# Kernel tuning notes

Measured on AMD Instinct MI355X. Metric: run time of the kernel, lower is better.

Reference implementation:

```python
import jax, jax.numpy as jnp
import numpy as np

DECAY = 0.8
CODEBOOK_SIZE = 1024
DIM = 128


def setup_inputs() -> dict:
    key = jax.random.key(0)
    k1, k2 = jax.random.split(key)
    x = jax.random.normal(k1, (16, 4096, DIM), dtype=jnp.float32)
    embed = jax.random.normal(k2, (CODEBOOK_SIZE, DIM), dtype=jnp.float32)
    ema_embed = embed * 1.0  # ema_num_initial = 1.0
    ema_num = jnp.ones((CODEBOOK_SIZE,), dtype=jnp.float32)
    return {"x": x, "embed": embed, "ema_embed": ema_embed, "ema_num": ema_num}


def reference(x, embed, ema_embed, ema_num):
    # flatten: [..., d] -> [N, d]
    shape = x.shape
    flatten = x.reshape(-1, shape[-1])  # [N, d]
    distance = -2.0 * (flatten @ embed.T) + jnp.sum(embed * embed, axis=-1)  # [N, K]
    embed_ind = jnp.argmin(distance, axis=-1)  # [N]
    quantize = embed[embed_ind.reshape(shape[:-1])]  # gather -> [..., d]

    # training branch: onehot^T @ flatten == segment_sum over code indices
    num_curr = jax.ops.segment_sum(
        jnp.ones_like(embed_ind, dtype=jnp.float32), embed_ind,
        num_segments=CODEBOOK_SIZE)  # [K]
    embed_curr = jax.ops.segment_sum(
        flatten.astype(jnp.float32), embed_ind,
        num_segments=CODEBOOK_SIZE)  # [K, d]

    ema_num_new = ema_num * DECAY + (1.0 - DECAY) * num_curr
    ema_embed_new = ema_embed * DECAY + (1.0 - DECAY) * embed_curr
    embed_new = ema_embed_new / ema_num_new[:, None]
    return quantize, embed_new, ema_embed_new, ema_num_new
```

## Files before the change

### kernel.cpp

```cpp
#include <hip/hip_runtime.h>

#define NPTS    65536
#define DIM     128
#define KCODES  1024
#define BM      64
#define TILE_C  64
#define NTHR    256
#define NTILE   (KCODES / TILE_C)

typedef _Float16 f16x8 __attribute__((ext_vector_type(8)));
typedef float    f32x4 __attribute__((ext_vector_type(4)));

__device__ __forceinline__ void gload_lds16(const void* g, void* l) {
    __builtin_amdgcn_global_load_lds(
        (const __attribute__((address_space(1))) void*)g,
        (__attribute__((address_space(3))) void*)l, 16, 0, 0);
}

__global__ __launch_bounds__(256)
void pack_kernel(const float* __restrict__ embed, _Float16* __restrict__ ebf,
                 int* __restrict__ ghist, int* __restrict__ gcursor,
                 const float* __restrict__ ema_embed, float* __restrict__ acc,
                 float* __restrict__ hn)
{
    __shared__ float partial[256];
    const int t = threadIdx.x;
    const int b = blockIdx.x;
    const int g = b * 256 + t;
    if (g < KCODES) { ghist[g] = 0; gcursor[g] = 0; }
    {
        float4 e0 = reinterpret_cast<const float4*>(ema_embed)[g];
        float4 e1 = reinterpret_cast<const float4*>(ema_embed)[g + 16384];
        reinterpret_cast<float4*>(acc)[g] =
            (float4){0.8f * e0.x, 0.8f * e0.y, 0.8f * e0.z, 0.8f * e0.w};
        reinterpret_cast<float4*>(acc)[g + 16384] =
            (float4){0.8f * e1.x, 0.8f * e1.y, 0.8f * e1.z, 0.8f * e1.w};
    }

    const int tc  = g >> 10;
    const int f   = (g >> 6) & 15;
    const int l   = g & 63;
    const int nt  = f >> 2;
    const int akk = f & 3;
    const int hg  = l >> 4;
    const int n   = l & 15;
    const int c   = tc * TILE_C + nt * 16 + n;
    const int d0  = akk * 32 + hg * 8;
    const float* src = embed + (long)c * DIM + d0;
    float4 v0 = *reinterpret_cast<const float4*>(src);
    float4 v1 = *reinterpret_cast<const float4*>(src + 4);
    float vv[8] = {v0.x, v0.y, v0.z, v0.w, v1.x, v1.y, v1.z, v1.w};
    f16x8 out;
    float ss = 0.f;
    #pragma unroll
    for (int j = 0; j < 8; ++j) {
        _Float16 h = (_Float16)vv[j];
        out[j] = h;
        float r = (float)h;
        ss += r * r;
    }
    *reinterpret_cast<f16x8*>(ebf + (long)g * 8) = out;

    partial[t] = ss;
    __syncthreads();
    if (t < 16) {
        float s = 0.f;
        #pragma unroll
        for (int k = 0; k < 16; ++k) s += partial[t + k * 16];
        hn[(b >> 2) * TILE_C + (b & 3) * 16 + t] = 0.5f * s;
    }
}

__global__ __launch_bounds__(NTHR, 4)
void argmin_kernel(const float* __restrict__ x, const _Float16* __restrict__ ebf,
                   const float* __restrict__ halfnorm, const float* __restrict__ embed,
                   int* __restrict__ ind, float* __restrict__ quant,
                   int* __restrict__ ghist)
{
    __shared__ _Float16 es[2][8192];
    __shared__ int      hist[KCODES];
    __shared__ int      bidx[BM];

    const int t    = threadIdx.x;
    const int lane = t & 63;
    const int w    = t >> 6;
    const int r16  = lane & 15;
    const int h4   = lane >> 4;
    const long xbase = (long)blockIdx.x * BM * DIM;
    const int  wp    = w * 16;

    for (int i = t; i < KCODES; i += NTHR) hist[i] = 0;

    f16x8 a[4];
    {
        const long prow = xbase + (long)(wp + r16) * DIM;
        #pragma unroll
        for (int akk = 0; akk < 4; ++akk) {
            const float* s = x + prow + akk * 32 + h4 * 8;
            float4 u0 = *reinterpret_cast<const float4*>(s);
            float4 u1 = *reinterpret_cast<const float4*>(s + 4);
            float vv[8] = {u0.x, u0.y, u0.z, u0.w, u1.x, u1.y, u1.z, u1.w};
            #pragma unroll
            for (int j = 0; j < 8; ++j) a[akk][j] = (_Float16)vv[j];
        }
    }

    #pragma unroll
    for (int i = 0; i < 4; ++i) {
        const int f = w * 4 + i;
        gload_lds16(ebf + (long)f * 512 + lane * 8, &es[0][f * 512]);
    }
    float hnv_cur[4], hnv_nxt[4];
    #pragma unroll
    for (int nt = 0; nt < 4; ++nt) hnv_cur[nt] = halfnorm[nt * 16 + r16];
    __syncthreads();

    float bestv[4];
    int   besti[4];
    #pragma unroll
    for (int s = 0; s < 4; ++s) { bestv[s] = -1e30f; besti[s] = 0; }

    #pragma unroll 1
    for (int tile = 0; tile < NTILE; ++tile) {
        if (tile + 1 < NTILE) {
            const long gbase = (long)(tile + 1) * 8192;
            #pragma unroll
            for (int i = 0; i < 4; ++i) {
                const int f = w * 4 + i;
                gload_lds16(ebf + gbase + f * 512 + lane * 8, &es[(tile + 1) & 1][f * 512]);
            }
            #pragma unroll
            for (int nt = 0; nt < 4; ++nt)
                hnv_nxt[nt] = halfnorm[(tile + 1) * TILE_C + nt * 16 + r16];
        }

        f32x4 C[4];
        #pragma unroll
        for (int nt = 0; nt < 4; ++nt) C[nt] = (f32x4){0.f, 0.f, 0.f, 0.f};

        #pragma unroll
        for (int akk = 0; akk < 4; ++akk) {
            #pragma unroll
            for (int nt = 0; nt < 4; ++nt) {
                f16x8 B = *reinterpret_cast<const f16x8*>(
                    &es[tile & 1][(nt * 4 + akk) * 512 + lane * 8]);
                C[nt] = __builtin_amdgcn_mfma_f32_16x16x32_f16(a[akk], B, C[nt], 0, 0, 0);
            }
        }

        #pragma unroll
        for (int nt = 0; nt < 4; ++nt) {
            const int c = tile * TILE_C + nt * 16 + r16;
            #pragma unroll
            for (int reg = 0; reg < 4; ++reg) {
                float sc = C[nt][reg] - hnv_cur[nt];
                if (sc > bestv[reg]) { bestv[reg] = sc; besti[reg] = c; }
            }
        }
        #pragma unroll
        for (int nt = 0; nt < 4; ++nt) hnv_cur[nt] = hnv_nxt[nt];
        __syncthreads();
    }

    #pragma unroll
    for (int s = 0; s < 4; ++s) {
        float v = bestv[s];
        int   i = besti[s];
        #pragma unroll
        for (int off = 1; off < 16; off <<= 1) {
            float ov = __shfl_xor(v, off);
            int   oi = __shfl_xor(i, off);
            if (ov > v || (ov == v && oi < i)) { v = ov; i = oi; }
        }
        bestv[s] = v; besti[s] = i;
    }
    if (r16 == 0) {
        #pragma unroll
        for (int s = 0; s < 4; ++s) {
            int p = wp + h4 * 4 + s;
            bidx[p] = besti[s];
            ind[blockIdx.x * BM + p] = besti[s];
        }
    }
    __syncthreads();

    if (t < BM) atomicAdd(&hist[bidx[t]], 1);

    float4* dst = reinterpret_cast<float4*>(quant + xbase);
    #pragma unroll
    for (int i = 0; i < 8; ++i) {
        int idx = i * NTHR + t;
        int p   = idx >> 5;
        int q   = idx & 31;
        int c   = bidx[p];
        dst[idx] = reinterpret_cast<const float4*>(embed + (long)c * DIM)[q];
    }

    __syncthreads();
    for (int i = t; i < KCODES; i += NTHR)
        if (hist[i]) atomicAdd(&ghist[i], hist[i]);
}

__global__ __launch_bounds__(256)
void scatter_kernel(const int* __restrict__ ghist, const int* __restrict__ ind,
                    const float* __restrict__ ema_num, float* __restrict__ ema_num_new,
                    int* __restrict__ gcursor, int* __restrict__ sorted,
                    int* __restrict__ scode)
{
    __shared__ int off_lds[KCODES];
    __shared__ int wsum[4];
    const int t    = threadIdx.x;
    const int lane = t & 63;
    const int w    = t >> 6;

    int v[4], pre[4];
    int s = 0;
    #pragma unroll
    for (int j = 0; j < 4; ++j) {
        v[j] = ghist[t * 4 + j];
        pre[j] = s;
        s += v[j];
    }
    int incl = s;
    #pragma unroll
    for (int off = 1; off < 64; off <<= 1) {
        int u = __shfl_up(incl, off);
        if (lane >= off) incl += u;
    }
    if (lane == 63) wsum[w] = incl;
    __syncthreads();
    if (t == 0) {
        int a = 0;
        #pragma unroll
        for (int k = 0; k < 4; ++k) { int tmp = wsum[k]; wsum[k] = a; a += tmp; }
    }
    __syncthreads();
    const int excl = wsum[w] + incl - s;
    #pragma unroll
    for (int j = 0; j < 4; ++j) off_lds[t * 4 + j] = excl + pre[j];

    if (blockIdx.x == 0) {
        #pragma unroll
        for (int j = 0; j < 4; ++j)
            ema_num_new[t * 4 + j] = ema_num[t * 4 + j] * 0.8f + 0.2f * (float)v[j];
    }
    __syncthreads();

    const int p = blockIdx.x * 256 + t;
    const int c = ind[p];
    const int pos = off_lds[c] + atomicAdd(&gcursor[c], 1);
    sorted[pos] = p;
    scode[pos]  = c;
}

__global__ __launch_bounds__(128)
void sum2_kernel(const float* __restrict__ x, const int* __restrict__ sorted,
                 const int* __restrict__ scode, float* __restrict__ acc)
{
    __shared__ int sp[64];
    __shared__ int sc[64];
    const int t = threadIdx.x;
    const int base = blockIdx.x * 64;
    if (t < 64) { sp[t] = sorted[base + t]; sc[t] = scode[base + t]; }
    __syncthreads();

    float a = 0.f;
    int cprev = sc[0];
    #pragma unroll 1
    for (int kk = 0; kk < 8; ++kk) {
        float v[8];
        #pragma unroll
        for (int i = 0; i < 8; ++i)
            v[i] = x[(long)sp[kk * 8 + i] * DIM + t];
        #pragma unroll
        for (int i = 0; i < 8; ++i) {
            const int c = sc[kk * 8 + i];
            if (c != cprev) {
                atomicAdd(&acc[(long)cprev * DIM + t], 0.2f * a);
                a = 0.f; cprev = c;
            }
            a += v[i];
        }
    }
    atomicAdd(&acc[(long)cprev * DIM + t], 0.2f * a);
}

__global__ __launch_bounds__(256)
void final_kernel(const float* __restrict__ acc, const float* __restrict__ ema_num_new,
                  float* __restrict__ embed_new)
{
    const int g = blockIdx.x * 256 + threadIdx.x;
    float4 v = reinterpret_cast<const float4*>(acc)[g];
    const float en = ema_num_new[g >> 5];
    float4 o = {v.x / en, v.y / en, v.z / en, v.w / en};
    reinterpret_cast<float4*>(embed_new)[g] = o;
}

extern "C" void kernel_launch(void* const* d_in, const int* in_sizes, int n_in,
                              void* d_out, int out_size, void* d_ws, size_t ws_size,
                              hipStream_t stream)
{
    const float* x         = (const float*)d_in[0];
    const float* embed     = (const float*)d_in[1];
    const float* ema_embed = (const float*)d_in[2];
    const float* ema_num   = (const float*)d_in[3];

    float* out0 = (float*)d_out;
    float* out1 = out0 + 8388608;
    float* out2 = out1 + 131072;
    float* out3 = out2 + 131072;

    char* ws = (char*)d_ws;
    float*    hn      = (float*)ws;
    int*      ind     = (int*)(ws + 4096);
    _Float16* ebf     = (_Float16*)(ws + 266240);
    int*      ghist   = (int*)(ws + 528384);
    int*      gcursor = (int*)(ws + 532480);
    int*      sorted  = (int*)(ws + 536576);
    int*      scode   = (int*)(ws + 798720);

    pack_kernel<<<64, 256, 0, stream>>>(embed, ebf, ghist, gcursor, ema_embed,
                                        out2, hn);
    argmin_kernel<<<NPTS / BM, NTHR, 0, stream>>>(x, ebf, hn, embed, ind, out0, ghist);
    scatter_kernel<<<NPTS / 256, 256, 0, stream>>>(ghist, ind, ema_num, out3,
                                                   gcursor, sorted, scode);
    sum2_kernel<<<NPTS / 64, 128, 0, stream>>>(x, sorted, scode, out2);
    final_kernel<<<128, 256, 0, stream>>>(out2, out3, out1);
}
```

Baseline: 95.96 us.

## Switch argmin GEMM to 32x32x16 MFMA with 128-row blocks

Replaces the 16x16x32 f16 MFMA tiles with 32x32x16 tiles, giving each wave 32 points and doubling the block to 128 rows. The packed codebook layout and the half-norm computation in the pack kernel are reworked to match. This halves how often each codebook tile is reloaded from LDS per point and cuts the number of blocks, but raises register use (16 accumulators plus 16 best values and indices), so launch bounds drop to 2 blocks per SIMD. The row-to-index mapping of the reduction changes accordingly, and a wrong mapping would give incorrect indices.

```diff
diff --git a/kernel.cpp b/kernel.cpp
--- a/kernel.cpp
+++ b/kernel.cpp
@@ -3,13 +3,13 @@
 #define NPTS    65536
 #define DIM     128
 #define KCODES  1024
-#define BM      64
+#define BM      128
 #define TILE_C  64
 #define NTHR    256
 #define NTILE   (KCODES / TILE_C)
 
-typedef _Float16 f16x8 __attribute__((ext_vector_type(8)));
-typedef float    f32x4 __attribute__((ext_vector_type(4)));
+typedef _Float16 f16x8  __attribute__((ext_vector_type(8)));
+typedef float    f32x16 __attribute__((ext_vector_type(16)));
 
 __device__ __forceinline__ void gload_lds16(const void* g, void* l) {
     __builtin_amdgcn_global_load_lds(
@@ -37,41 +37,49 @@
             (float4){0.8f * e1.x, 0.8f * e1.y, 0.8f * e1.z, 0.8f * e1.w};
     }
 
-    const int tc  = g >> 10;
-    const int f   = (g >> 6) & 15;
-    const int l   = g & 63;
-    const int nt  = f >> 2;
-    const int akk = f & 3;
-    const int hg  = l >> 4;
-    const int n   = l & 15;
-    const int c   = tc * TILE_C + nt * 16 + n;
-    const int d0  = akk * 32 + hg * 8;
-    const float* src = embed + (long)c * DIM + d0;
-    float4 v0 = *reinterpret_cast<const float4*>(src);
-    float4 v1 = *reinterpret_cast<const float4*>(src + 4);
-    float vv[8] = {v0.x, v0.y, v0.z, v0.w, v1.x, v1.y, v1.z, v1.w};
-    f16x8 out;
-    float ss = 0.f;
-    #pragma unroll
-    for (int j = 0; j < 8; ++j) {
-        _Float16 h = (_Float16)vv[j];
-        out[j] = h;
-        float r = (float)h;
-        ss += r * r;
-    }
-    *reinterpret_cast<f16x8*>(ebf + (long)g * 8) = out;
-
-    partial[t] = ss;
-    __syncthreads();
-    if (t < 16) {
-        float s = 0.f;
-        #pragma unroll
-        for (int k = 0; k < 16; ++k) s += partial[t + k * 16];
-        hn[(b >> 2) * TILE_C + (b & 3) * 16 + t] = 0.5f * s;
-    }
-}
-
-__global__ __launch_bounds__(NTHR, 4)
+    {
+        const int tc  = g >> 10;
+        const int f   = (g >> 6) & 15;
+        const int l   = g & 63;
+        const int nt  = f >> 3;
+        const int kc  = f & 7;
+        const int c   = tc * TILE_C + nt * 32 + (l & 31);
+        const int d0  = kc * 16 + (l >> 5) * 8;
+        const float* src = embed + (long)c * DIM + d0;
+        float4 v0 = *reinterpret_cast<const float4*>(src);
+        float4 v1 = *reinterpret_cast<const float4*>(src + 4);
+        float vv[8] = {v0.x, v0.y, v0.z, v0.w, v1.x, v1.y, v1.z, v1.w};
+        f16x8 out;
+        #pragma unroll
+        for (int j = 0; j < 8; ++j) out[j] = (_Float16)vv[j];
+        *reinterpret_cast<f16x8*>(ebf + (long)g * 8) = out;
+    }
+
+    {
+        const int c2    = b * 16 + (t >> 4);
+        const int chunk = t & 15;
+        const float* src = embed + (long)c2 * DIM + chunk * 8;
+        float4 v0 = *reinterpret_cast<const float4*>(src);
+        float4 v1 = *reinterpret_cast<const float4*>(src + 4);
+        float vv[8] = {v0.x, v0.y, v0.z, v0.w, v1.x, v1.y, v1.z, v1.w};
+        float ss = 0.f;
+        #pragma unroll
+        for (int j = 0; j < 8; ++j) {
+            float r = (float)(_Float16)vv[j];
+            ss += r * r;
+        }
+        partial[t] = ss;
+        __syncthreads();
+        if ((t & 15) == 0) {
+            float s = 0.f;
+            #pragma unroll
+            for (int j = 0; j < 16; ++j) s += partial[t + j];
+            hn[c2] = 0.5f * s;
+        }
+    }
+}
+
+__global__ __launch_bounds__(NTHR, 2)
 void argmin_kernel(const float* __restrict__ x, const _Float16* __restrict__ ebf,
                    const float* __restrict__ halfnorm, const float* __restrict__ embed,
                    int* __restrict__ ind, float* __restrict__ quant,
@@ -84,24 +92,24 @@
     const int t    = threadIdx.x;
     const int lane = t & 63;
     const int w    = t >> 6;
-    const int r16  = lane & 15;
-    const int h4   = lane >> 4;
+    const int r32  = lane & 31;
+    const int ksub = lane >> 5;
     const long xbase = (long)blockIdx.x * BM * DIM;
-    const int  wp    = w * 16;
+    const int  wp    = w * 32;
 
     for (int i = t; i < KCODES; i += NTHR) hist[i] = 0;
 
-    f16x8 a[4];
+    f16x8 a[8];
     {
-        const long prow = xbase + (long)(wp + r16) * DIM;
-        #pragma unroll
-        for (int akk = 0; akk < 4; ++akk) {
-            const float* s = x + prow + akk * 32 + h4 * 8;
+        const long prow = xbase + (long)(wp + r32) * DIM;
+        #pragma unroll
+        for (int kc = 0; kc < 8; ++kc) {
+            const float* s = x + prow + kc * 16 + ksub * 8;
             float4 u0 = *reinterpret_cast<const float4*>(s);
             float4 u1 = *reinterpret_cast<const float4*>(s + 4);
             float vv[8] = {u0.x, u0.y, u0.z, u0.w, u1.x, u1.y, u1.z, u1.w};
             #pragma unroll
-            for (int j = 0; j < 8; ++j) a[akk][j] = (_Float16)vv[j];
+            for (int j = 0; j < 8; ++j) a[kc][j] = (_Float16)vv[j];
         }
     }
 
@@ -110,15 +118,15 @@
         const int f = w * 4 + i;
         gload_lds16(ebf + (long)f * 512 + lane * 8, &es[0][f * 512]);
     }
-    float hnv_cur[4], hnv_nxt[4];
-    #pragma unroll
-    for (int nt = 0; nt < 4; ++nt) hnv_cur[nt] = halfnorm[nt * 16 + r16];
-    __syncthreads();
-
-    float bestv[4];
-    int   besti[4];
-    #pragma unroll
-    for (int s = 0; s < 4; ++s) { bestv[s] = -1e30f; besti[s] = 0; }
+    float hnv_cur[2], hnv_nxt[2];
+    #pragma unroll
+    for (int nt = 0; nt < 2; ++nt) hnv_cur[nt] = halfnorm[nt * 32 + r32];
+    __syncthreads();
+
+    float bestv[16];
+    int   besti[16];
+    #pragma unroll
+    for (int s = 0; s < 16; ++s) { bestv[s] = -1e30f; besti[s] = 0; }
 
     #pragma unroll 1
     for (int tile = 0; tile < NTILE; ++tile) {
@@ -130,54 +138,49 @@
                 gload_lds16(ebf + gbase + f * 512 + lane * 8, &es[(tile + 1) & 1][f * 512]);
             }
             #pragma unroll
-            for (int nt = 0; nt < 4; ++nt)
-                hnv_nxt[nt] = halfnorm[(tile + 1) * TILE_C + nt * 16 + r16];
-        }
-
-        f32x4 C[4];
-        #pragma unroll
-        for (int nt = 0; nt < 4; ++nt) C[nt] = (f32x4){0.f, 0.f, 0.f, 0.f};
-
-        #pragma unroll
-        for (int akk = 0; akk < 4; ++akk) {
-            #pragma unroll
-            for (int nt = 0; nt < 4; ++nt) {
+            for (int nt = 0; nt < 2; ++nt)
+                hnv_nxt[nt] = halfnorm[(tile + 1) * TILE_C + nt * 32 + r32];
+        }
+
+        #pragma unroll
+        for (int nt = 0; nt < 2; ++nt) {
+            f32x16 C = {0.f, 0.f, 0.f, 0.f, 0.f, 0.f, 0.f, 0.f,
+                        0.f, 0.f, 0.f, 0.f, 0.f, 0.f, 0.f, 0.f};
+            #pragma unroll
+            for (int kc = 0; kc < 8; ++kc) {
                 f16x8 B = *reinterpret_cast<const f16x8*>(
-                    &es[tile & 1][(nt * 4 + akk) * 512 + lane * 8]);
-                C[nt] = __builtin_amdgcn_mfma_f32_16x16x32_f16(a[akk], B, C[nt], 0, 0, 0);
+                    &es[tile & 1][(nt * 8 + kc) * 512 + lane * 8]);
+                C = __builtin_amdgcn_mfma_f32_32x32x16_f16(a[kc], B, C, 0, 0, 0);
             }
-        }
-
-        #pragma unroll
-        for (int nt = 0; nt < 4; ++nt) {
-            const int c = tile * TILE_C + nt * 16 + r16;
-            #pragma unroll
-            for (int reg = 0; reg < 4; ++reg) {
-                float sc = C[nt][reg] - hnv_cur[nt];
+            const int c = tile * TILE_C + nt * 32 + r32;
+            const float hnv = hnv_cur[nt];
+            #pragma unroll
+            for (int reg = 0; reg < 16; ++reg) {
+                float sc = C[reg] - hnv;
                 if (sc > bestv[reg]) { bestv[reg] = sc; besti[reg] = c; }
             }
         }
-        #pragma unroll
-        for (int nt = 0; nt < 4; ++nt) hnv_cur[nt] = hnv_nxt[nt];
+        hnv_cur[0] = hnv_nxt[0];
+        hnv_cur[1] = hnv_nxt[1];
         __syncthreads();
     }
 
     #pragma unroll
-    for (int s = 0; s < 4; ++s) {
+    for (int s = 0; s < 16; ++s) {
         float v = bestv[s];
         int   i = besti[s];
         #pragma unroll
-        for (int off = 1; off < 16; off <<= 1) {
+        for (int off = 1; off < 32; off <<= 1) {
             float ov = __shfl_xor(v, off);
             int   oi = __shfl_xor(i, off);
             if (ov > v || (ov == v && oi < i)) { v = ov; i = oi; }
         }
         bestv[s] = v; besti[s] = i;
     }
-    if (r16 == 0) {
-        #pragma unroll
-        for (int s = 0; s < 4; ++s) {
-            int p = wp + h4 * 4 + s;
+    if (r32 == 0) {
+        #pragma unroll
+        for (int s = 0; s < 16; ++s) {
+            int p = wp + (s & 3) + 8 * (s >> 2) + 4 * ksub;
             bidx[p] = besti[s];
             ind[blockIdx.x * BM + p] = besti[s];
         }
@@ -188,7 +191,7 @@
 
     float4* dst = reinterpret_cast<float4*>(quant + xbase);
     #pragma unroll
-    for (int i = 0; i < 8; ++i) {
+    for (int i = 0; i < 16; ++i) {
         int idx = i * NTHR + t;
         int p   = idx >> 5;
         int q   = idx & 31;
```

Measured after the change: 97.03 us. No clear change (+1.1%).

## Fuse EMA embedding accumulation into argmin via direct atomics, drop sort kernels

Applied to the files above, without the earlier changes.

Removes the counting-sort scatter kernel and the segmented-sum kernel. The argmin kernel now atomically adds each point's scaled features into its assigned code's accumulator while the x tile is hot. ema_num_new is computed in the final kernel from the histogram. This trades launch overhead and an extra pass over x plus the sort traffic for one float atomic per element, with nondeterministic summation order and possible atomic contention.

```diff
diff --git a/kernel.cpp b/kernel.cpp
--- a/kernel.cpp
+++ b/kernel.cpp
@@ -19,15 +19,14 @@
 
 __global__ __launch_bounds__(256)
 void pack_kernel(const float* __restrict__ embed, _Float16* __restrict__ ebf,
-                 int* __restrict__ ghist, int* __restrict__ gcursor,
-                 const float* __restrict__ ema_embed, float* __restrict__ acc,
-                 float* __restrict__ hn)
+                 int* __restrict__ ghist, const float* __restrict__ ema_embed,
+                 float* __restrict__ acc, float* __restrict__ hn)
 {
     __shared__ float partial[256];
     const int t = threadIdx.x;
     const int b = blockIdx.x;
     const int g = b * 256 + t;
-    if (g < KCODES) { ghist[g] = 0; gcursor[g] = 0; }
+    if (g < KCODES) ghist[g] = 0;
     {
         float4 e0 = reinterpret_cast<const float4*>(ema_embed)[g];
         float4 e1 = reinterpret_cast<const float4*>(ema_embed)[g + 16384];
@@ -74,8 +73,8 @@
 __global__ __launch_bounds__(NTHR, 4)
 void argmin_kernel(const float* __restrict__ x, const _Float16* __restrict__ ebf,
                    const float* __restrict__ halfnorm, const float* __restrict__ embed,
-                   int* __restrict__ ind, float* __restrict__ quant,
-                   int* __restrict__ ghist)
+                   float* __restrict__ quant, int* __restrict__ ghist,
+                   float* __restrict__ acc)
 {
     __shared__ _Float16 es[2][8192];
     __shared__ int      hist[KCODES];
@@ -179,7 +178,6 @@
         for (int s = 0; s < 4; ++s) {
             int p = wp + h4 * 4 + s;
             bidx[p] = besti[s];
-            ind[blockIdx.x * BM + p] = besti[s];
         }
     }
     __syncthreads();
@@ -199,99 +197,27 @@
     __syncthreads();
     for (int i = t; i < KCODES; i += NTHR)
         if (hist[i]) atomicAdd(&ghist[i], hist[i]);
+
+    #pragma unroll 4
+    for (int rep = 0; rep < BM * DIM / NTHR; ++rep) {
+        const int flat = rep * NTHR + t;
+        const int p    = flat >> 7;
+        const int d    = flat & 127;
+        atomicAdd(&acc[(long)bidx[p] * DIM + d],
+                  0.2f * x[xbase + (long)p * DIM + d]);
+    }
 }
 
 __global__ __launch_bounds__(256)
-void scatter_kernel(const int* __restrict__ ghist, const int* __restrict__ ind,
-                    const float* __restrict__ ema_num, float* __restrict__ ema_num_new,
-                    int* __restrict__ gcursor, int* __restrict__ sorted,
-                    int* __restrict__ scode)
-{
-    __shared__ int off_lds[KCODES];
-    __shared__ int wsum[4];
-    const int t    = threadIdx.x;
-    const int lane = t & 63;
-    const int w    = t >> 6;
-
-    int v[4], pre[4];
-    int s = 0;
-    #pragma unroll
-    for (int j = 0; j < 4; ++j) {
-        v[j] = ghist[t * 4 + j];
-        pre[j] = s;
-        s += v[j];
-    }
-    int incl = s;
-    #pragma unroll
-    for (int off = 1; off < 64; off <<= 1) {
-        int u = __shfl_up(incl, off);
-        if (lane >= off) incl += u;
-    }
-    if (lane == 63) wsum[w] = incl;
-    __syncthreads();
-    if (t == 0) {
-        int a = 0;
-        #pragma unroll
-        for (int k = 0; k < 4; ++k) { int tmp = wsum[k]; wsum[k] = a; a += tmp; }
-    }
-    __syncthreads();
-    const int excl = wsum[w] + incl - s;
-    #pragma unroll
-    for (int j = 0; j < 4; ++j) off_lds[t * 4 + j] = excl + pre[j];
-
-    if (blockIdx.x == 0) {
-        #pragma unroll
-        for (int j = 0; j < 4; ++j)
-            ema_num_new[t * 4 + j] = ema_num[t * 4 + j] * 0.8f + 0.2f * (float)v[j];
-    }
-    __syncthreads();
-
-    const int p = blockIdx.x * 256 + t;
-    const int c = ind[p];
-    const int pos = off_lds[c] + atomicAdd(&gcursor[c], 1);
-    sorted[pos] = p;
-    scode[pos]  = c;
-}
-
-__global__ __launch_bounds__(128)
-void sum2_kernel(const float* __restrict__ x, const int* __restrict__ sorted,
-                 const int* __restrict__ scode, float* __restrict__ acc)
-{
-    __shared__ int sp[64];
-    __shared__ int sc[64];
-    const int t = threadIdx.x;
-    const int base = blockIdx.x * 64;
-    if (t < 64) { sp[t] = sorted[base + t]; sc[t] = scode[base + t]; }
-    __syncthreads();
-
-    float a = 0.f;
-    int cprev = sc[0];
-    #pragma unroll 1
-    for (int kk = 0; kk < 8; ++kk) {
-        float v[8];
-        #pragma unroll
-        for (int i = 0; i < 8; ++i)
-            v[i] = x[(long)sp[kk * 8 + i] * DIM + t];
-        #pragma unroll
-        for (int i = 0; i < 8; ++i) {
-            const int c = sc[kk * 8 + i];
-            if (c != cprev) {
-                atomicAdd(&acc[(long)cprev * DIM + t], 0.2f * a);
-                a = 0.f; cprev = c;
-            }
-            a += v[i];
-        }
-    }
-    atomicAdd(&acc[(long)cprev * DIM + t], 0.2f * a);
-}
-
-__global__ __launch_bounds__(256)
-void final_kernel(const float* __restrict__ acc, const float* __restrict__ ema_num_new,
+void final_kernel(const float* __restrict__ acc, const int* __restrict__ ghist,
+                  const float* __restrict__ ema_num, float* __restrict__ ema_num_new,
                   float* __restrict__ embed_new)
 {
     const int g = blockIdx.x * 256 + threadIdx.x;
+    const int c = g >> 5;
     float4 v = reinterpret_cast<const float4*>(acc)[g];
-    const float en = ema_num_new[g >> 5];
+    const float en = ema_num[c] * 0.8f + 0.2f * (float)ghist[c];
+    if ((g & 31) == 0) ema_num_new[c] = en;
     float4 o = {v.x / en, v.y / en, v.z / en, v.w / en};
     reinterpret_cast<float4*>(embed_new)[g] = o;
 }
@@ -311,19 +237,11 @@
     float* out3 = out2 + 131072;
 
     char* ws = (char*)d_ws;
-    float*    hn      = (float*)ws;
-    int*      ind     = (int*)(ws + 4096);
-    _Float16* ebf     = (_Float16*)(ws + 266240);
-    int*      ghist   = (int*)(ws + 528384);
-    int*      gcursor = (int*)(ws + 532480);
-    int*      sorted  = (int*)(ws + 536576);
-    int*      scode   = (int*)(ws + 798720);
-
-    pack_kernel<<<64, 256, 0, stream>>>(embed, ebf, ghist, gcursor, ema_embed,
-                                        out2, hn);
-    argmin_kernel<<<NPTS / BM, NTHR, 0, stream>>>(x, ebf, hn, embed, ind, out0, ghist);
-    scatter_kernel<<<NPTS / 256, 256, 0, stream>>>(ghist, ind, ema_num, out3,
-                                                   gcursor, sorted, scode);
-    sum2_kernel<<<NPTS / 64, 128, 0, stream>>>(x, sorted, scode, out2);
-    final_kernel<<<128, 256, 0, stream>>>(out2, out3, out1);
-}
+    float*    hn    = (float*)ws;
+    _Float16* ebf   = (_Float16*)(ws + 4096);
+    int*      ghist = (int*)(ws + 266240);
+
+    pack_kernel<<<64, 256, 0, stream>>>(embed, ebf, ghist, ema_embed, out2, hn);
+    argmin_kernel<<<NPTS / BM, NTHR, 0, stream>>>(x, ebf, hn, embed, out0, ghist, out2);
+    final_kernel<<<128, 256, 0, stream>>>(out2, ghist, ema_num, out3, out1);
+}
```

Result: slower. 119.8 us (+24.9%).

## Fuse argmin, scatter, segment-sum and finalize into one cooperative kernel

Applied to the files above, without the earlier changes.

Replaces the four kernels after packing with a single cooperative kernel that uses grid-wide syncs between the argmin, prefix-scan/scatter, sorted segment-sum and final EMA division phases. Blocks double to 128 points and 512 threads, giving 512 blocks so the grid can be co-resident. The goal is to cut launch gaps and inter-kernel drain time. In exchange it pays for three grid barriers and needs every block resident at once, and it falls back to the multi-kernel path if the cooperative launch fails.

```diff
diff --git a/kernel.cpp b/kernel.cpp
--- a/kernel.cpp
+++ b/kernel.cpp
@@ -1,12 +1,16 @@
 #include <hip/hip_runtime.h>
+#include <hip/hip_cooperative_groups.h>
+
+namespace cg = cooperative_groups;
 
 #define NPTS    65536
 #define DIM     128
 #define KCODES  1024
-#define BM      64
+#define BM      128
 #define TILE_C  64
-#define NTHR    256
+#define NTHR    512
 #define NTILE   (KCODES / TILE_C)
+#define NBLK    (NPTS / BM)
 
 typedef _Float16 f16x8 __attribute__((ext_vector_type(8)));
 typedef float    f32x4 __attribute__((ext_vector_type(4)));
@@ -71,22 +75,20 @@
     }
 }
 
-__global__ __launch_bounds__(NTHR, 4)
-void argmin_kernel(const float* __restrict__ x, const _Float16* __restrict__ ebf,
-                   const float* __restrict__ halfnorm, const float* __restrict__ embed,
-                   int* __restrict__ ind, float* __restrict__ quant,
-                   int* __restrict__ ghist)
-{
-    __shared__ _Float16 es[2][8192];
-    __shared__ int      hist[KCODES];
-    __shared__ int      bidx[BM];
-
+__device__ __forceinline__
+void argmin_phase(const float* __restrict__ x, const _Float16* __restrict__ ebf,
+                  const float* __restrict__ halfnorm, const float* __restrict__ embed,
+                  int* __restrict__ ind, float* __restrict__ quant,
+                  int* __restrict__ ghist,
+                  _Float16 (*es)[8192], int* hist, int* bidx)
+{
     const int t    = threadIdx.x;
     const int lane = t & 63;
     const int w    = t >> 6;
     const int r16  = lane & 15;
     const int h4   = lane >> 4;
-    const long xbase = (long)blockIdx.x * BM * DIM;
+    const int blk  = blockIdx.x;
+    const long xbase = (long)blk * BM * DIM;
     const int  wp    = w * 16;
 
     for (int i = t; i < KCODES; i += NTHR) hist[i] = 0;
@@ -106,8 +108,8 @@
     }
 
     #pragma unroll
-    for (int i = 0; i < 4; ++i) {
-        const int f = w * 4 + i;
+    for (int i = 0; i < 2; ++i) {
+        const int f = w * 2 + i;
         gload_lds16(ebf + (long)f * 512 + lane * 8, &es[0][f * 512]);
     }
     float hnv_cur[4], hnv_nxt[4];
@@ -125,8 +127,8 @@
         if (tile + 1 < NTILE) {
             const long gbase = (long)(tile + 1) * 8192;
             #pragma unroll
-            for (int i = 0; i < 4; ++i) {
-                const int f = w * 4 + i;
+            for (int i = 0; i < 2; ++i) {
+                const int f = w * 2 + i;
                 gload_lds16(ebf + gbase + f * 512 + lane * 8, &es[(tile + 1) & 1][f * 512]);
             }
             #pragma unroll
@@ -179,26 +181,151 @@
         for (int s = 0; s < 4; ++s) {
             int p = wp + h4 * 4 + s;
             bidx[p] = besti[s];
-            ind[blockIdx.x * BM + p] = besti[s];
+            ind[blk * BM + p] = besti[s];
         }
     }
     __syncthreads();
 
     if (t < BM) atomicAdd(&hist[bidx[t]], 1);
 
-    float4* dst = reinterpret_cast<float4*>(quant + xbase);
-    #pragma unroll
-    for (int i = 0; i < 8; ++i) {
-        int idx = i * NTHR + t;
-        int p   = idx >> 5;
-        int q   = idx & 31;
-        int c   = bidx[p];
-        dst[idx] = reinterpret_cast<const float4*>(embed + (long)c * DIM)[q];
+    {
+        float4* dst = reinterpret_cast<float4*>(quant + xbase);
+        #pragma unroll
+        for (int i = 0; i < 8; ++i) {
+            int idx = i * NTHR + t;
+            int p   = idx >> 5;
+            int q   = idx & 31;
+            int c   = bidx[p];
+            dst[idx] = reinterpret_cast<const float4*>(embed + (long)c * DIM)[q];
+        }
     }
 
     __syncthreads();
     for (int i = t; i < KCODES; i += NTHR)
         if (hist[i]) atomicAdd(&ghist[i], hist[i]);
+}
+
+__global__ __launch_bounds__(NTHR, 4)
+void fused_kernel(const float* __restrict__ x, const _Float16* __restrict__ ebf,
+                  const float* __restrict__ halfnorm, const float* __restrict__ embed,
+                  const float* __restrict__ ema_num,
+                  float* __restrict__ quant, float* __restrict__ embed_new,
+                  float* __restrict__ acc ,
+                  float* __restrict__ ema_num_new,
+                  int* __restrict__ ind, int* __restrict__ ghist,
+                  int* __restrict__ gcursor, int* __restrict__ sorted,
+                  int* __restrict__ scode)
+{
+    cg::grid_group grid = cg::this_grid();
+
+    __shared__ _Float16 es[2][8192];
+    __shared__ int      hist[KCODES];
+    __shared__ int      bidx[BM];
+    __shared__ int      wsum[8];
+
+    const int t    = threadIdx.x;
+    const int lane = t & 63;
+    const int w    = t >> 6;
+    const int blk  = blockIdx.x;
+
+    argmin_phase(x, ebf, halfnorm, embed, ind, quant, ghist, es, hist, bidx);
+
+    grid.sync();
+
+    {
+        int* off_lds = reinterpret_cast<int*>(&es[0][0]);
+        int v[2], pre[2];
+        int s = 0;
+        #pragma unroll
+        for (int j = 0; j < 2; ++j) {
+            v[j] = ghist[t * 2 + j];
+            pre[j] = s;
+            s += v[j];
+        }
+        int incl = s;
+        #pragma unroll
+        for (int off = 1; off < 64; off <<= 1) {
+            int u = __shfl_up(incl, off);
+            if (lane >= off) incl += u;
+        }
+        if (lane == 63) wsum[w] = incl;
+        __syncthreads();
+        if (t == 0) {
+            int aa = 0;
+            #pragma unroll
+            for (int k = 0; k < 8; ++k) { int tmp = wsum[k]; wsum[k] = aa; aa += tmp; }
+        }
+        __syncthreads();
+        const int excl = wsum[w] + incl - s;
+        #pragma unroll
+        for (int j = 0; j < 2; ++j) off_lds[t * 2 + j] = excl + pre[j];
+        __syncthreads();
+
+        if (t < BM) {
+            const int p = blk * BM + t;
+            const int c = bidx[t];
+            const int pos = off_lds[c] + atomicAdd(&gcursor[c], 1);
+            sorted[pos] = p;
+            scode[pos]  = c;
+        }
+    }
+
+    grid.sync();
+
+    {
+        int* sp = hist;
+        int* sc = hist + 128;
+        const int base = blk * BM;
+        __syncthreads();
+        if (t < BM) { sp[t] = sorted[base + t]; sc[t] = scode[base + t]; }
+        __syncthreads();
+
+        if (t < 256) {
+            const int d   = t & 127;
+            const int sb  = (t >> 7) * 64;
+            float aa = 0.f;
+            int cprev = sc[sb];
+            #pragma unroll 1
+            for (int kk = 0; kk < 8; ++kk) {
+                float vv[8];
+                #pragma unroll
+                for (int i = 0; i < 8; ++i)
+                    vv[i] = x[(long)sp[sb + kk * 8 + i] * DIM + d];
+                #pragma unroll
+                for (int i = 0; i < 8; ++i) {
+                    const int c = sc[sb + kk * 8 + i];
+                    if (c != cprev) {
+                        atomicAdd(&acc[(long)cprev * DIM + d], 0.2f * aa);
+                        aa = 0.f; cprev = c;
+                    }
+                    aa += vv[i];
+                }
+            }
+            atomicAdd(&acc[(long)cprev * DIM + d], 0.2f * aa);
+        }
+    }
+
+    grid.sync();
+
+    if (t < 256) {
+        const int c = blk * 2 + (t >> 7);
+        const int d = t & 127;
+        const float en = ema_num[c] * 0.8f + 0.2f * (float)ghist[c];
+        embed_new[(long)c * DIM + d] = acc[(long)c * DIM + d] / en;
+        if (d == 0) ema_num_new[c] = en;
+    }
+}
+
+__global__ __launch_bounds__(NTHR, 4)
+void argmin_fb(const float* __restrict__ x, const _Float16* __restrict__ ebf,
+               const float* __restrict__ halfnorm, const float* __restrict__ embed,
+               int* __restrict__ ind, float* __restrict__ quant,
+               int* __restrict__ ghist)
+{
+    __shared__ _Float16 es[2][8192];
+    __shared__ int      hist[KCODES];
+    __shared__ int      bidx[BM];
+    argmin_phase(x, ebf, halfnorm, embed, ind, quant, ghist, es, hist, bidx);
 }
 
 __global__ __launch_bounds__(256)
@@ -312,18 +439,28 @@
 
     char* ws = (char*)d_ws;
     float*    hn      = (float*)ws;
-    int*      ind     = (int*)(ws + 4096);
-    _Float16* ebf     = (_Float16*)(ws + 266240);
-    int*      ghist   = (int*)(ws + 528384);
-    int*      gcursor = (int*)(ws + 532480);
+    _Float16* ebf     = (_Float16*)(ws + 4096);
+    int*      ghist   = (int*)(ws + 266240);
+    int*      gcursor = (int*)(ws + 270336);
+    int*      ind     = (int*)(ws + 274432);
     int*      sorted  = (int*)(ws + 536576);
     int*      scode   = (int*)(ws + 798720);
 
     pack_kernel<<<64, 256, 0, stream>>>(embed, ebf, ghist, gcursor, ema_embed,
                                         out2, hn);
-    argmin_kernel<<<NPTS / BM, NTHR, 0, stream>>>(x, ebf, hn, embed, ind, out0, ghist);
-    scatter_kernel<<<NPTS / 256, 256, 0, stream>>>(ghist, ind, ema_num, out3,
-                                                   gcursor, sorted, scode);
-    sum2_kernel<<<NPTS / 64, 128, 0, stream>>>(x, sorted, scode, out2);
-    final_kernel<<<128, 256, 0, stream>>>(out2, out3, out1);
-}
+
+    void* args[] = {
+        (void*)&x, (void*)&ebf, (void*)&hn, (void*)&embed, (void*)&ema_num,
+        (void*)&out0, (void*)&out1, (void*)&out2, (void*)&out3,
+        (void*)&ind, (void*)&ghist, (void*)&gcursor, (void*)&sorted, (void*)&scode
+    };
+    hipError_t err = hipLaunchCooperativeKernel((const void*)fused_kernel,
+                                                dim3(NBLK), dim3(NTHR), args, 0, stream);
+    if (err != hipSuccess) {
+        argmin_fb<<<NBLK, NTHR, 0, stream>>>(x, ebf, hn, embed, ind, out0, ghist);
+        scatter_kernel<<<NPTS / 256, 256, 0, stream>>>(ghist, ind, ema_num, out3,
+                                                       gcursor, sorted, scode);
+        sum2_kernel<<<NPTS / 64, 128, 0, stream>>>(x, sorted, scode, out2);
+        final_kernel<<<128, 256, 0, stream>>>(out2, out3, out1);
+    }
+}
```

After: 272.5 us. 184% more time.
